# Kernel tuning notes

Measured on AMD Instinct MI355X. Metric: run time of the kernel, lower is better.

## Reference

```python
import jax, jax.numpy as jnp
import numpy as np

NEG_SLOPE = 0.2

def edge_softmax(logits, dst, num_nodes):
    # logits: [E, H]; softmax over incoming edges of each dst node, per head
    m = jax.ops.segment_max(logits, dst, num_segments=num_nodes)  # [N, H]
    e = jnp.exp(logits - m[dst])
    s = jax.ops.segment_sum(e, dst, num_segments=num_nodes)  # [N, H]
    return e / s[dst]

def gat_layer(h, src, dst, W, al, ar, b, activation):
    # W: [F_in, H*D], al/ar: [H, D], b: [H, D]
    N = h.shape[0]
    H, D = al.shape
    feat = (h @ W).reshape(N, H, D)
    el = jnp.sum(feat * al, axis=-1)  # [N, H]
    er = jnp.sum(feat * ar, axis=-1)  # [N, H]
    e = jax.nn.leaky_relu(el[src] + er[dst], NEG_SLOPE)  # [E, H]
    a = edge_softmax(e, dst, N)  # [E, H]
    msg = feat[src] * a[:, :, None]  # [E, H, D]
    rst = jax.ops.segment_sum(msg, dst, num_segments=N) + b[None]  # [N, H, D]
    if activation:
        rst = jax.nn.relu(rst)
    return rst

def setup_inputs() -> dict:
    key = jax.random.key(0)
    ks = jax.random.split(key, 16)
    N, E = 50000, 800000
    IN, HID, OUT, H = 128, 64, 64, 4
    s = 0.1
    return {
        "features": jax.random.normal(ks[0], (N, IN), jnp.float32),
        "src": jax.random.randint(ks[1], (E,), 0, N),
        "dst": jax.random.randint(ks[2], (E,), 0, N),
        "W1": jax.random.normal(ks[3], (IN, H * HID), jnp.float32) * s,
        "al1": jax.random.normal(ks[4], (H, HID), jnp.float32) * s,
        "ar1": jax.random.normal(ks[5], (H, HID), jnp.float32) * s,
        "b1": jnp.zeros((H, HID), jnp.float32),
        "W2": jax.random.normal(ks[6], (H * HID, H * HID), jnp.float32) * s,
        "al2": jax.random.normal(ks[7], (H, HID), jnp.float32) * s,
        "ar2": jax.random.normal(ks[8], (H, HID), jnp.float32) * s,
        "b2": jnp.zeros((H, HID), jnp.float32),
        "W3": jax.random.normal(ks[9], (H * HID, OUT), jnp.float32) * s,
        "al3": jax.random.normal(ks[10], (1, OUT), jnp.float32) * s,
        "ar3": jax.random.normal(ks[11], (1, OUT), jnp.float32) * s,
        "b3": jnp.zeros((1, OUT), jnp.float32),
    }

def reference(features, src, dst, W1, al1, ar1, b1, W2, al2, ar2, b2, W3, al3, ar3, b3):
    N = features.shape[0]
    h = gat_layer(features, src, dst, W1, al1, ar1, b1, activation=True)   # [N, 4, 64]
    h = h.reshape(N, -1)                                                    # [N, 256]
    h = gat_layer(h, src, dst, W2, al2, ar2, b2, activation=True)          # [N, 4, 64]
    h = h.reshape(N, -1)                                                    # [N, 256]
    h = gat_layer(h, src, dst, W3, al3, ar3, b3, activation=False)         # [N, 1, 64]
    return h.mean(axis=1)                                                   # [N, 64]
```

## Files before the change

### kernel.cpp

```cpp
#include <hip/hip_runtime.h>
#include <hip/hip_bf16.h>

#define LEAKY 0.2f

typedef __attribute__((ext_vector_type(8))) short short8;
typedef __attribute__((ext_vector_type(4))) float f32x4;

__device__ inline unsigned short f2b(float f) {
    unsigned u = __float_as_uint(f);
    u += 0x7FFFu + ((u >> 16) & 1u);
    return (unsigned short)(u >> 16);
}
__device__ inline float b2f(unsigned short s) {
    return __uint_as_float(((unsigned)s) << 16);
}


__global__ void k_prep(const float* __restrict__ features, unsigned short* __restrict__ fconv,
                       int n4,
                       const float* __restrict__ W1, const float* __restrict__ W2,
                       const float* __restrict__ W3, unsigned short* __restrict__ Wt1,
                       unsigned short* __restrict__ Wt2, unsigned short* __restrict__ Wt3,
                       int* __restrict__ bcnt) {
    int idx = blockIdx.x * blockDim.x + threadIdx.x;
    if (idx < n4) {
        float4 v = *(const float4*)(features + idx * 4);
        ushort4 o;
        o.x = f2b(v.x); o.y = f2b(v.y); o.z = f2b(v.z); o.w = f2b(v.w);
        *(ushort4*)(fconv + idx * 4) = o;
        return;
    }
    int j = idx - n4;
    if (j < 32768) {
        int m = j >> 7, k = j & 127;
        Wt1[j] = f2b(W1[(size_t)k * 256 + m]);
        return;
    }
    if (j < 98304) {
        int jj = j - 32768;
        int m = jj >> 8, k = jj & 255;
        Wt2[jj] = f2b(W2[(size_t)k * 256 + m]);
        return;
    }
    if (j < 114688) {
        int jj = j - 98304;
        int m = jj >> 8, k = jj & 255;
        Wt3[jj] = f2b(W3[(size_t)k * 64 + m]);
        return;
    }
    int z = j - 114688;
    if (z < 256) bcnt[z] = 0;
}


#define NEB 8192

__global__ __launch_bounds__(256)
void k_bin_count(const int* __restrict__ dst, int* __restrict__ bcnt, int E, int N) {
    __shared__ int lc[256];
    const int tid = threadIdx.x;
    lc[tid] = 0;
    __syncthreads();
    const int b0 = blockIdx.x * NEB;
    const int cnt = min(NEB, E - b0);
    for (int j = 0; j < NEB / 256; ++j) {
        int idx = j * 256 + tid;
        if (idx < cnt) {
            int dn = dst[b0 + idx];
            if ((unsigned)dn < (unsigned)N) atomicAdd(&lc[dn >> 8], 1);
        }
    }
    __syncthreads();
    if (lc[tid] > 0) atomicAdd(&bcnt[tid], lc[tid]);
}

__global__ __launch_bounds__(256)
void k_bucket_scan(const int* __restrict__ bcnt, int* __restrict__ bbase,
                   int* __restrict__ bcur, int* __restrict__ row_start_N, int B, int E) {
    __shared__ int ws[4];
    const int tid = threadIdx.x, lane = tid & 63, wave = tid >> 6;
    int v = (tid < B) ? bcnt[tid] : 0;
    int x = v;
    #pragma unroll
    for (int off = 1; off < 64; off <<= 1) {
        int t = __shfl_up(x, off, 64);
        if (lane >= off) x += t;
    }
    if (lane == 63) ws[wave] = x;
    __syncthreads();
    if (tid == 0) {
        int c = 0;
        #pragma unroll
        for (int wv = 0; wv < 4; ++wv) { int t = ws[wv]; ws[wv] = c; c += t; }
    }
    __syncthreads();
    int excl = x - v + ws[wave];
    if (tid < B) { bbase[tid] = excl; bcur[tid] = excl; }
    if (tid == 0) { bbase[B] = E; *row_start_N = E; }
}

__global__ __launch_bounds__(256)
void k_bin_scatter(const int* __restrict__ dst, int* __restrict__ bcur,
                   int* __restrict__ ebuf, int E, int N) {
    __shared__ int lc[256], lofs[256], lcur[256], gres[256];
    __shared__ int stage_e[NEB];
    __shared__ unsigned short stage_d[NEB];
    __shared__ int ws[4];
    const int tid = threadIdx.x, lane = tid & 63, wave = tid >> 6;
    const int b0 = blockIdx.x * NEB;
    const int cnt = min(NEB, E - b0);
    lc[tid] = 0;
    __syncthreads();

    int dreg[NEB / 256];
    #pragma unroll
    for (int j = 0; j < NEB / 256; ++j) {
        int idx = j * 256 + tid;
        dreg[j] = -1;
        if (idx < cnt) {
            int dn = dst[b0 + idx];
            if ((unsigned)dn < (unsigned)N) {
                dreg[j] = dn;
                atomicAdd(&lc[dn >> 8], 1);
            }
        }
    }
    __syncthreads();
    {
        int v = lc[tid];
        int x = v;
        #pragma unroll
        for (int off = 1; off < 64; off <<= 1) {
            int t = __shfl_up(x, off, 64);
            if (lane >= off) x += t;
        }
        if (lane == 63) ws[wave] = x;
        __syncthreads();
        if (tid == 0) {
            int c = 0;
            #pragma unroll
            for (int wv = 0; wv < 4; ++wv) { int t = ws[wv]; ws[wv] = c; c += t; }
        }
        __syncthreads();
        int excl = x - v + ws[wave];
        lofs[tid] = excl;
        lcur[tid] = excl;
    }
    __syncthreads();
    #pragma unroll
    for (int j = 0; j < NEB / 256; ++j) {
        int dn = dreg[j];
        if (dn >= 0) {
            int p = atomicAdd(&lcur[dn >> 8], 1);
            stage_e[p] = b0 + j * 256 + tid;
            stage_d[p] = (unsigned short)dn;
        }
    }
    __syncthreads();
    if (lc[tid] > 0) gres[tid] = atomicAdd(&bcur[tid], lc[tid]);
    __syncthreads();
    int total = lcur[255];
    for (int i = tid; i < total; i += 256) {
        int dn = stage_d[i];
        int k = dn >> 8;
        int dest = gres[k] + (i - lofs[k]);
        ebuf[dest] = ((dn & 255) << 24) | stage_e[i];
    }
}

__global__ __launch_bounds__(256)
void k_csr_build(const int* __restrict__ ebuf, const int* __restrict__ src,
                 const int* __restrict__ bbase, int* __restrict__ row_start,
                 int* __restrict__ src_sorted, int N) {
    __shared__ int lc[256], lcur[256];
    __shared__ int ws[4];
    const int tid = threadIdx.x, lane = tid & 63, wave = tid >> 6;
    const int k = blockIdx.x;
    const int base = k << 8;
    const int e0 = bbase[k];
    const int cnt = bbase[k + 1] - e0;
    lc[tid] = 0;
    __syncthreads();
    for (int i = tid; i < cnt; i += 256) {
        int rel = ((unsigned)ebuf[e0 + i]) >> 24;
        atomicAdd(&lc[rel], 1);
    }
    __syncthreads();
    {
        int v = lc[tid];
        int x = v;
        #pragma unroll
        for (int off = 1; off < 64; off <<= 1) {
            int t = __shfl_up(x, off, 64);
            if (lane >= off) x += t;
        }
        if (lane == 63) ws[wave] = x;
        __syncthreads();
        if (tid == 0) {
            int c = 0;
            #pragma unroll
            for (int wv = 0; wv < 4; ++wv) { int t = ws[wv]; ws[wv] = c; c += t; }
        }
        __syncthreads();
        int excl = x - v + ws[wave];
        lcur[tid] = excl;
        int n = base + tid;
        if (n < N) row_start[n] = e0 + excl;
    }
    __syncthreads();
    for (int i = tid; i < cnt; i += 256) {
        int val = ebuf[e0 + i];
        int rel = ((unsigned)val) >> 24;
        int e = val & 0xFFFFFF;
        int p = atomicAdd(&lcur[rel], 1);
        src_sorted[e0 + p] = src[e];
    }
}


__global__ __launch_bounds__(256)
void k_gemm_mfma(const unsigned short* __restrict__ A, const unsigned short* __restrict__ Wt,
                 unsigned short* __restrict__ Cb, const float* __restrict__ al,
                 const float* __restrict__ ar, float* __restrict__ el,
                 float* __restrict__ er, int N, int K, int M) {
    constexpr int STR = 40;
    __shared__ unsigned short As[128 * STR];
    __shared__ unsigned short Bs[128 * STR];
    const int tid  = threadIdx.x;
    const int wave = tid >> 6;
    const int lane = tid & 63;
    const int row0 = blockIdx.y * 128;
    const int col0 = blockIdx.x * 128;
    const int wr = (wave >> 1) * 64;
    const int wc = (wave & 1) * 64;
    const int m16 = lane & 15;
    const int q   = lane >> 4;

    const int s_row = tid >> 1;
    const int s_off = (tid & 1) * 16;

    f32x4 acc[4][4] = {};

    for (int k0 = 0; k0 < K; k0 += 32) {
        {
            int gr = row0 + s_row;
            short8 z = {};
            short8 v0 = z, v1 = z;
            if (gr < N) {
                const unsigned short* ap = A + (size_t)gr * K + k0 + s_off;
                v0 = *(const short8*)ap;
                v1 = *(const short8*)(ap + 8);
            }
            *(short8*)&As[s_row * STR + s_off]     = v0;
            *(short8*)&As[s_row * STR + s_off + 8] = v1;
        }
        {
            const unsigned short* sp = Wt + (size_t)(col0 + s_row) * K + k0 + s_off;
            *(short8*)&Bs[s_row * STR + s_off]     = *(const short8*)sp;
            *(short8*)&Bs[s_row * STR + s_off + 8] = *(const short8*)(sp + 8);
        }
        __syncthreads();

        short8 afr[4], bfr[4];
        #pragma unroll
        for (int rg = 0; rg < 4; ++rg)
            afr[rg] = *(const short8*)&As[(wr + rg * 16 + m16) * STR + q * 8];
        #pragma unroll
        for (int cg = 0; cg < 4; ++cg)
            bfr[cg] = *(const short8*)&Bs[(wc + cg * 16 + m16) * STR + q * 8];
        #pragma unroll
        for (int rg = 0; rg < 4; ++rg)
            #pragma unroll
            for (int cg = 0; cg < 4; ++cg)
                acc[rg][cg] = __builtin_amdgcn_mfma_f32_16x16x32_bf16(
                    afr[rg], bfr[cg], acc[rg][cg], 0, 0, 0);
        __syncthreads();
    }

    const int H = M >> 6;
    const int h = (col0 + wc) >> 6;
    float alv[4], arv[4];
    #pragma unroll
    for (int cg = 0; cg < 4; ++cg) {
        alv[cg] = al[h * 64 + cg * 16 + m16];
        arv[cg] = ar[h * 64 + cg * 16 + m16];
    }

    #pragma unroll
    for (int rg = 0; rg < 4; ++rg) {
        #pragma unroll
        for (int r = 0; r < 4; ++r) {
            int gr = row0 + wr + rg * 16 + q * 4 + r;
            float pl = 0.f, pr = 0.f;
            #pragma unroll
            for (int cg = 0; cg < 4; ++cg) {
                pl = fmaf(acc[rg][cg][r], alv[cg], pl);
                pr = fmaf(acc[rg][cg][r], arv[cg], pr);
            }
            #pragma unroll
            for (int off = 1; off < 16; off <<= 1) {
                pl += __shfl_xor(pl, off, 64);
                pr += __shfl_xor(pr, off, 64);
            }
            if (gr < N) {
                unsigned short* bp = Cb + (size_t)gr * M + col0 + wc + m16;
                #pragma unroll
                for (int cg = 0; cg < 4; ++cg)
                    bp[cg * 16] = f2b(acc[rg][cg][r]);
                if (m16 == 0) {
                    el[gr * H + h] = pl;
                    er[gr * H + h] = pr;
                }
            }
        }
    }
}


__global__ __launch_bounds__(256)
void k_gemm_mfma64(const unsigned short* __restrict__ A, const unsigned short* __restrict__ Wt,
                   unsigned short* __restrict__ Cb, const float* __restrict__ al,
                   const float* __restrict__ ar, float* __restrict__ el,
                   float* __restrict__ er, int N, int K) {
    constexpr int M = 64;
    constexpr int STR = 40;
    __shared__ unsigned short As[256 * STR];
    __shared__ unsigned short Bs[64 * STR];
    const int tid  = threadIdx.x;
    const int wave = tid >> 6;
    const int lane = tid & 63;
    const int row0 = blockIdx.x * 256;
    const int wr = wave * 64;
    const int m16 = lane & 15;
    const int q   = lane >> 4;

    const int s_row = tid >> 1;
    const int s_off = (tid & 1) * 16;
    const int b_row = tid >> 2;
    const int b_chk = (tid & 3) * 8;

    f32x4 acc[4][4] = {};

    for (int k0 = 0; k0 < K; k0 += 32) {
        #pragma unroll
        for (int p = 0; p < 2; ++p) {
            int r = s_row + p * 128;
            int gr = row0 + r;
            short8 z = {};
            short8 v0 = z, v1 = z;
            if (gr < N) {
                const unsigned short* ap = A + (size_t)gr * K + k0 + s_off;
                v0 = *(const short8*)ap;
                v1 = *(const short8*)(ap + 8);
            }
            *(short8*)&As[r * STR + s_off]     = v0;
            *(short8*)&As[r * STR + s_off + 8] = v1;
        }
        {
            const unsigned short* sp = Wt + (size_t)b_row * K + k0 + b_chk;
            *(short8*)&Bs[b_row * STR + b_chk] = *(const short8*)sp;
        }
        __syncthreads();

        short8 afr[4], bfr[4];
        #pragma unroll
        for (int rg = 0; rg < 4; ++rg)
            afr[rg] = *(const short8*)&As[(wr + rg * 16 + m16) * STR + q * 8];
        #pragma unroll
        for (int cg = 0; cg < 4; ++cg)
            bfr[cg] = *(const short8*)&Bs[(cg * 16 + m16) * STR + q * 8];
        #pragma unroll
        for (int rg = 0; rg < 4; ++rg)
            #pragma unroll
            for (int cg = 0; cg < 4; ++cg)
                acc[rg][cg] = __builtin_amdgcn_mfma_f32_16x16x32_bf16(
                    afr[rg], bfr[cg], acc[rg][cg], 0, 0, 0);
        __syncthreads();
    }

    float alv[4], arv[4];
    #pragma unroll
    for (int cg = 0; cg < 4; ++cg) {
        alv[cg] = al[cg * 16 + m16];
        arv[cg] = ar[cg * 16 + m16];
    }

    #pragma unroll
    for (int rg = 0; rg < 4; ++rg) {
        #pragma unroll
        for (int r = 0; r < 4; ++r) {
            int gr = row0 + wr + rg * 16 + q * 4 + r;
            float pl = 0.f, pr = 0.f;
            #pragma unroll
            for (int cg = 0; cg < 4; ++cg) {
                pl = fmaf(acc[rg][cg][r], alv[cg], pl);
                pr = fmaf(acc[rg][cg][r], arv[cg], pr);
            }
            #pragma unroll
            for (int off = 1; off < 16; off <<= 1) {
                pl += __shfl_xor(pl, off, 64);
                pr += __shfl_xor(pr, off, 64);
            }
            if (gr < N) {
                unsigned short* bp = Cb + (size_t)gr * M + m16;
                #pragma unroll
                for (int cg = 0; cg < 4; ++cg)
                    bp[cg * 16] = f2b(acc[rg][cg][r]);
                if (m16 == 0) {
                    el[gr] = pl;
                    er[gr] = pr;
                }
            }
        }
    }
}


template<int H>
__global__ __launch_bounds__(256)
void k_node_msw(const int* __restrict__ row_start, const int* __restrict__ src_sorted,
                const float* __restrict__ el, const float* __restrict__ er,
                float* __restrict__ w, unsigned short* __restrict__ wb,
                float* __restrict__ s, int N, int E) {
    constexpr int STRIDE = 64 / H;
    constexpr int CAP = 64;
    constexpr int LSTR = 65;
    __shared__ float ldsw[4 * H * LSTR];
    const int wv = threadIdx.x >> 6;
    const int n = blockIdx.x * 4 + wv;
    if (n >= N) return;
    const int lane = threadIdx.x & 63;
    const int eo = lane / H;
    const int h  = lane % H;
    float* lw = &ldsw[(wv * H + h) * LSTR];
    float erv = er[n * H + h];
    int b0 = row_start[n], b1 = row_start[n + 1];
    float mx = -INFINITY;
    for (int i = b0 + eo; i < b1; i += STRIDE) {
        float x = el[src_sorted[i] * H + h] + erv;
        x = (x > 0.f) ? x : LEAKY * x;
        int j = i - b0;
        if (j < CAP) lw[j] = x;
        else w[(size_t)h * E + i] = x;
        mx = fmaxf(mx, x);
    }
    #pragma unroll
    for (int off = H; off < 64; off <<= 1)
        mx = fmaxf(mx, __shfl_xor(mx, off, 64));
    float sum = 0.f;
    for (int i = b0 + eo; i < b1; i += STRIDE) {
        int j = i - b0;
        float x = (j < CAP) ? lw[j] : w[(size_t)h * E + i];
        float e = __expf(x - mx);
        sum += e;
        wb[(size_t)h * E + i] = f2b(e);
    }
    #pragma unroll
    for (int off = H; off < 64; off <<= 1)
        sum += __shfl_xor(sum, off, 64);
    if (lane < H) s[n * H + lane] = 1.0f / fmaxf(sum, 1e-30f);
}

template<int OUTBF>
__global__ __launch_bounds__(256)
void k_agg_b(const int* __restrict__ row_start, const int* __restrict__ src_sorted,
             const uint4* __restrict__ featp, const unsigned short* __restrict__ wb,
             const float* __restrict__ s, const float* __restrict__ bias,
             void* __restrict__ outv, int H, int N, int E, int do_relu) {
    const int M = H * 64;
    const int P = M >> 3;
    const int G = 256 / P;
    const int grp = threadIdx.x / P;
    const int t = threadIdx.x - grp * P;
    const int n = blockIdx.x * G + grp;
    if (n >= N) return;
    const int d0 = t * 8;
    const int h = d0 >> 6;
    const unsigned short* wh = wb + (size_t)h * E;

    float a[8] = {};
    int b0 = row_start[n], b1 = row_start[n + 1];
    int i = b0;
    for (; i + 8 <= b1; i += 8) {
        int ss[8]; float wv[8]; uint4 pv[8];
        #pragma unroll
        for (int j = 0; j < 8; ++j) ss[j] = src_sorted[i + j];
        #pragma unroll
        for (int j = 0; j < 8; ++j) wv[j] = b2f(wh[i + j]);
        #pragma unroll
        for (int j = 0; j < 8; ++j) pv[j] = featp[(size_t)ss[j] * P + t];
        #pragma unroll
        for (int j = 0; j < 8; ++j) {
            a[0] = fmaf(__uint_as_float(pv[j].x << 16),         wv[j], a[0]);
            a[1] = fmaf(__uint_as_float(pv[j].x & 0xFFFF0000u), wv[j], a[1]);
            a[2] = fmaf(__uint_as_float(pv[j].y << 16),         wv[j], a[2]);
            a[3] = fmaf(__uint_as_float(pv[j].y & 0xFFFF0000u), wv[j], a[3]);
            a[4] = fmaf(__uint_as_float(pv[j].z << 16),         wv[j], a[4]);
            a[5] = fmaf(__uint_as_float(pv[j].z & 0xFFFF0000u), wv[j], a[5]);
            a[6] = fmaf(__uint_as_float(pv[j].w << 16),         wv[j], a[6]);
            a[7] = fmaf(__uint_as_float(pv[j].w & 0xFFFF0000u), wv[j], a[7]);
        }
    }
    for (; i + 4 <= b1; i += 4) {
        int ss[4]; float wv[4]; uint4 pv[4];
        #pragma unroll
        for (int j = 0; j < 4; ++j) ss[j] = src_sorted[i + j];
        #pragma unroll
        for (int j = 0; j < 4; ++j) wv[j] = b2f(wh[i + j]);
        #pragma unroll
        for (int j = 0; j < 4; ++j) pv[j] = featp[(size_t)ss[j] * P + t];
        #pragma unroll
        for (int j = 0; j < 4; ++j) {
            a[0] = fmaf(__uint_as_float(pv[j].x << 16),         wv[j], a[0]);
            a[1] = fmaf(__uint_as_float(pv[j].x & 0xFFFF0000u), wv[j], a[1]);
            a[2] = fmaf(__uint_as_float(pv[j].y << 16),         wv[j], a[2]);
            a[3] = fmaf(__uint_as_float(pv[j].y & 0xFFFF0000u), wv[j], a[3]);
            a[4] = fmaf(__uint_as_float(pv[j].z << 16),         wv[j], a[4]);
            a[5] = fmaf(__uint_as_float(pv[j].z & 0xFFFF0000u), wv[j], a[5]);
            a[6] = fmaf(__uint_as_float(pv[j].w << 16),         wv[j], a[6]);
            a[7] = fmaf(__uint_as_float(pv[j].w & 0xFFFF0000u), wv[j], a[7]);
        }
    }
    for (; i < b1; ++i) {
        uint4 pv = featp[(size_t)src_sorted[i] * P + t];
        float wv = b2f(wh[i]);
        a[0] = fmaf(__uint_as_float(pv.x << 16),         wv, a[0]);
        a[1] = fmaf(__uint_as_float(pv.x & 0xFFFF0000u), wv, a[1]);
        a[2] = fmaf(__uint_as_float(pv.y << 16),         wv, a[2]);
        a[3] = fmaf(__uint_as_float(pv.y & 0xFFFF0000u), wv, a[3]);
        a[4] = fmaf(__uint_as_float(pv.z << 16),         wv, a[4]);
        a[5] = fmaf(__uint_as_float(pv.z & 0xFFFF0000u), wv, a[5]);
        a[6] = fmaf(__uint_as_float(pv.w << 16),         wv, a[6]);
        a[7] = fmaf(__uint_as_float(pv.w & 0xFFFF0000u), wv, a[7]);
    }
    float rs = s[n * H + h];
    float4 bv0 = *(const float4*)(bias + d0);
    float4 bv1 = *(const float4*)(bias + d0 + 4);
    a[0] = fmaf(a[0], rs, bv0.x); a[1] = fmaf(a[1], rs, bv0.y);
    a[2] = fmaf(a[2], rs, bv0.z); a[3] = fmaf(a[3], rs, bv0.w);
    a[4] = fmaf(a[4], rs, bv1.x); a[5] = fmaf(a[5], rs, bv1.y);
    a[6] = fmaf(a[6], rs, bv1.z); a[7] = fmaf(a[7], rs, bv1.w);
    if (do_relu) {
        #pragma unroll
        for (int j = 0; j < 8; ++j) a[j] = fmaxf(a[j], 0.f);
    }
    if (OUTBF) {
        uint4 o;
        o.x = (unsigned)f2b(a[0]) | ((unsigned)f2b(a[1]) << 16);
        o.y = (unsigned)f2b(a[2]) | ((unsigned)f2b(a[3]) << 16);
        o.z = (unsigned)f2b(a[4]) | ((unsigned)f2b(a[5]) << 16);
        o.w = (unsigned)f2b(a[6]) | ((unsigned)f2b(a[7]) << 16);
        *(uint4*)((unsigned short*)outv + (size_t)n * M + d0) = o;
    } else {
        *(float4*)((float*)outv + (size_t)n * M + d0)     = make_float4(a[0], a[1], a[2], a[3]);
        *(float4*)((float*)outv + (size_t)n * M + d0 + 4) = make_float4(a[4], a[5], a[6], a[7]);
    }
}


static void run_layer(const unsigned short* A, int K, const unsigned short* Wt,
                      const float* al_, const float* ar_, const float* b_, int H,
                      unsigned short* featb, void* rstOut, bool outBf,
                      float* el, float* er, float* w, unsigned short* wb, float* s,
                      const int* row_start, const int* src_sorted,
                      int N, int E, bool do_relu, hipStream_t stream) {
    const int M = H * 64;
    if (M % 128 == 0) {
        dim3 gg(M / 128, (N + 127) / 128);
        k_gemm_mfma<<<gg, 256, 0, stream>>>(A, Wt, featb, al_, ar_, el, er, N, K, M);
    } else {
        k_gemm_mfma64<<<(N + 255) / 256, 256, 0, stream>>>(A, Wt, featb, al_, ar_, el, er, N, K);
    }

    if (H == 4)
        k_node_msw<4><<<(N + 3) / 4, 256, 0, stream>>>(row_start, src_sorted, el, er, w, wb, s, N, E);
    else
        k_node_msw<1><<<(N + 3) / 4, 256, 0, stream>>>(row_start, src_sorted, el, er, w, wb, s, N, E);

    int G = 256 / (M / 8);
    if (outBf)
        k_agg_b<1><<<(N + G - 1) / G, 256, 0, stream>>>(row_start, src_sorted,
                                                        (const uint4*)featb, wb, s,
                                                        b_, rstOut, H, N, E, do_relu ? 1 : 0);
    else
        k_agg_b<0><<<(N + G - 1) / G, 256, 0, stream>>>(row_start, src_sorted,
                                                        (const uint4*)featb, wb, s,
                                                        b_, rstOut, H, N, E, do_relu ? 1 : 0);
}

extern "C" void kernel_launch(void* const* d_in, const int* in_sizes, int n_in,
                              void* d_out, int out_size, void* d_ws, size_t ws_size,
                              hipStream_t stream) {
    const float* features = (const float*)d_in[0];
    const int*   src = (const int*)d_in[1];
    const int*   dst = (const int*)d_in[2];
    const float* W1  = (const float*)d_in[3];
    const float* al1 = (const float*)d_in[4];
    const float* ar1 = (const float*)d_in[5];
    const float* b1  = (const float*)d_in[6];
    const float* W2  = (const float*)d_in[7];
    const float* al2 = (const float*)d_in[8];
    const float* ar2 = (const float*)d_in[9];
    const float* b2  = (const float*)d_in[10];
    const float* W3  = (const float*)d_in[11];
    const float* al3 = (const float*)d_in[12];
    const float* ar3 = (const float*)d_in[13];
    const float* b3  = (const float*)d_in[14];

    const int N = in_sizes[0] / 128;
    const int E = in_sizes[1];
    const int B = (N + 255) >> 8;
    const int n4 = N * 128 / 4;

    float* ws   = (float*)d_ws;
    float* el   = ws;
    float* er   = el + (size_t)N * 4;
    float* s    = er + (size_t)N * 4;
    float* w    = s  + (size_t)N * 4;
    unsigned short* wb = (unsigned short*)(w + (size_t)E * 4);
    int* row_start  = (int*)(wb + (size_t)E * 4);
    int* src_sorted = row_start + N + 1;
    int* ebuf       = src_sorted + E;
    int* bcnt       = ebuf + E;
    int* bbase      = bcnt + 256;
    int* bcur       = bbase + 257;
    uintptr_t wp = (uintptr_t)(bcur + 256);
    wp = (wp + 15) & ~(uintptr_t)15;
    unsigned short* Wt1   = (unsigned short*)wp;
    unsigned short* Wt2   = Wt1 + 32768;
    unsigned short* Wt3   = Wt2 + 65536;
    unsigned short* fconv = Wt3 + 16384;
    unsigned short* featb = fconv + (size_t)N * 128;
    unsigned short* rstb  = featb + (size_t)N * 256;

    int prep_total = n4 + 114688 + 256;
    k_prep<<<(prep_total + 255) / 256, 256, 0, stream>>>(features, fconv, n4,
                                                         W1, W2, W3, Wt1, Wt2, Wt3, bcnt);

    int nbb = (E + NEB - 1) / NEB;
    k_bin_count<<<nbb, 256, 0, stream>>>(dst, bcnt, E, N);
    k_bucket_scan<<<1, 256, 0, stream>>>(bcnt, bbase, bcur, row_start + N, B, E);
    k_bin_scatter<<<nbb, 256, 0, stream>>>(dst, bcur, ebuf, E, N);
    k_csr_build<<<B, 256, 0, stream>>>(ebuf, src, bbase, row_start, src_sorted, N);

    run_layer(fconv, 128, Wt1, al1, ar1, b1, 4, featb, rstb, true,
              el, er, w, wb, s, row_start, src_sorted, N, E, true, stream);
    run_layer(rstb, 256, Wt2, al2, ar2, b2, 4, featb, rstb, true,
              el, er, w, wb, s, row_start, src_sorted, N, E, true, stream);
    run_layer(rstb, 256, Wt3, al3, ar3, b3, 1, featb, d_out, false,
              el, er, w, wb, s, row_start, src_sorted, N, E, false, stream);
}
```

Before: 422.3 us.

## Fuse edge softmax into aggregation kernel using monotone max of el

Removes the separate per-node softmax kernel and computes the max from the max of el over incoming edges plus er, passed through leaky-relu, which is exact by monotonicity. The aggregation kernel now gathers el, computes the exp weights and their sum inline, and normalizes at the end. This eliminates the intermediate weight and inverse-sum buffers and one launch per layer. In exchange, every thread in a node group recomputes the exps, and el is gathered twice.

```diff
diff --git a/kernel.cpp b/kernel.cpp
--- a/kernel.cpp
+++ b/kernel.cpp
@@ -415,58 +415,12 @@
     }
 }
 
-
-template<int H>
-__global__ __launch_bounds__(256)
-void k_node_msw(const int* __restrict__ row_start, const int* __restrict__ src_sorted,
-                const float* __restrict__ el, const float* __restrict__ er,
-                float* __restrict__ w, unsigned short* __restrict__ wb,
-                float* __restrict__ s, int N, int E) {
-    constexpr int STRIDE = 64 / H;
-    constexpr int CAP = 64;
-    constexpr int LSTR = 65;
-    __shared__ float ldsw[4 * H * LSTR];
-    const int wv = threadIdx.x >> 6;
-    const int n = blockIdx.x * 4 + wv;
-    if (n >= N) return;
-    const int lane = threadIdx.x & 63;
-    const int eo = lane / H;
-    const int h  = lane % H;
-    float* lw = &ldsw[(wv * H + h) * LSTR];
-    float erv = er[n * H + h];
-    int b0 = row_start[n], b1 = row_start[n + 1];
-    float mx = -INFINITY;
-    for (int i = b0 + eo; i < b1; i += STRIDE) {
-        float x = el[src_sorted[i] * H + h] + erv;
-        x = (x > 0.f) ? x : LEAKY * x;
-        int j = i - b0;
-        if (j < CAP) lw[j] = x;
-        else w[(size_t)h * E + i] = x;
-        mx = fmaxf(mx, x);
-    }
-    #pragma unroll
-    for (int off = H; off < 64; off <<= 1)
-        mx = fmaxf(mx, __shfl_xor(mx, off, 64));
-    float sum = 0.f;
-    for (int i = b0 + eo; i < b1; i += STRIDE) {
-        int j = i - b0;
-        float x = (j < CAP) ? lw[j] : w[(size_t)h * E + i];
-        float e = __expf(x - mx);
-        sum += e;
-        wb[(size_t)h * E + i] = f2b(e);
-    }
-    #pragma unroll
-    for (int off = H; off < 64; off <<= 1)
-        sum += __shfl_xor(sum, off, 64);
-    if (lane < H) s[n * H + lane] = 1.0f / fmaxf(sum, 1e-30f);
-}
-
 template<int OUTBF>
 __global__ __launch_bounds__(256)
-void k_agg_b(const int* __restrict__ row_start, const int* __restrict__ src_sorted,
-             const uint4* __restrict__ featp, const unsigned short* __restrict__ wb,
-             const float* __restrict__ s, const float* __restrict__ bias,
-             void* __restrict__ outv, int H, int N, int E, int do_relu) {
+void k_agg_f(const int* __restrict__ row_start, const int* __restrict__ src_sorted,
+             const uint4* __restrict__ featp, const float* __restrict__ el,
+             const float* __restrict__ er, const float* __restrict__ bias,
+             void* __restrict__ outv, int H, int N, int do_relu) {
     const int M = H * 64;
     const int P = M >> 3;
     const int G = 256 / P;
@@ -476,19 +430,38 @@
     if (n >= N) return;
     const int d0 = t * 8;
     const int h = d0 >> 6;
-    const unsigned short* wh = wb + (size_t)h * E;
+    const float erv = er[n * H + h];
+
+    const int b0 = row_start[n], b1 = row_start[n + 1];
+
+    float mxe = -INFINITY;
+    for (int i = b0 + (t & 7); i < b1; i += 8)
+        mxe = fmaxf(mxe, el[(size_t)src_sorted[i] * H + h]);
+    mxe = fmaxf(mxe, __shfl_xor(mxe, 1, 64));
+    mxe = fmaxf(mxe, __shfl_xor(mxe, 2, 64));
+    mxe = fmaxf(mxe, __shfl_xor(mxe, 4, 64));
+    float mx = mxe + erv;
+    mx = (mx > 0.f) ? mx : LEAKY * mx;
 
     float a[8] = {};
-    int b0 = row_start[n], b1 = row_start[n + 1];
+    float sum = 0.f;
     int i = b0;
     for (; i + 8 <= b1; i += 8) {
         int ss[8]; float wv[8]; uint4 pv[8];
         #pragma unroll
         for (int j = 0; j < 8; ++j) ss[j] = src_sorted[i + j];
         #pragma unroll
-        for (int j = 0; j < 8; ++j) wv[j] = b2f(wh[i + j]);
+        for (int j = 0; j < 8; ++j) wv[j] = el[(size_t)ss[j] * H + h];
         #pragma unroll
         for (int j = 0; j < 8; ++j) pv[j] = featp[(size_t)ss[j] * P + t];
+        #pragma unroll
+        for (int j = 0; j < 8; ++j) {
+            float x = wv[j] + erv;
+            x = (x > 0.f) ? x : LEAKY * x;
+            float w = __expf(x - mx);
+            wv[j] = w;
+            sum += w;
+        }
         #pragma unroll
         for (int j = 0; j < 8; ++j) {
             a[0] = fmaf(__uint_as_float(pv[j].x << 16),         wv[j], a[0]);
@@ -506,9 +479,17 @@
         #pragma unroll
         for (int j = 0; j < 4; ++j) ss[j] = src_sorted[i + j];
         #pragma unroll
-        for (int j = 0; j < 4; ++j) wv[j] = b2f(wh[i + j]);
+        for (int j = 0; j < 4; ++j) wv[j] = el[(size_t)ss[j] * H + h];
         #pragma unroll
         for (int j = 0; j < 4; ++j) pv[j] = featp[(size_t)ss[j] * P + t];
+        #pragma unroll
+        for (int j = 0; j < 4; ++j) {
+            float x = wv[j] + erv;
+            x = (x > 0.f) ? x : LEAKY * x;
+            float w = __expf(x - mx);
+            wv[j] = w;
+            sum += w;
+        }
         #pragma unroll
         for (int j = 0; j < 4; ++j) {
             a[0] = fmaf(__uint_as_float(pv[j].x << 16),         wv[j], a[0]);
@@ -522,18 +503,23 @@
         }
     }
     for (; i < b1; ++i) {
-        uint4 pv = featp[(size_t)src_sorted[i] * P + t];
-        float wv = b2f(wh[i]);
-        a[0] = fmaf(__uint_as_float(pv.x << 16),         wv, a[0]);
-        a[1] = fmaf(__uint_as_float(pv.x & 0xFFFF0000u), wv, a[1]);
-        a[2] = fmaf(__uint_as_float(pv.y << 16),         wv, a[2]);
-        a[3] = fmaf(__uint_as_float(pv.y & 0xFFFF0000u), wv, a[3]);
-        a[4] = fmaf(__uint_as_float(pv.z << 16),         wv, a[4]);
-        a[5] = fmaf(__uint_as_float(pv.z & 0xFFFF0000u), wv, a[5]);
-        a[6] = fmaf(__uint_as_float(pv.w << 16),         wv, a[6]);
-        a[7] = fmaf(__uint_as_float(pv.w & 0xFFFF0000u), wv, a[7]);
-    }
-    float rs = s[n * H + h];
+        int ss = src_sorted[i];
+        float x = el[(size_t)ss * H + h] + erv;
+        uint4 pv = featp[(size_t)ss * P + t];
+        x = (x > 0.f) ? x : LEAKY * x;
+        float w = __expf(x - mx);
+        sum += w;
+        a[0] = fmaf(__uint_as_float(pv.x << 16),         w, a[0]);
+        a[1] = fmaf(__uint_as_float(pv.x & 0xFFFF0000u), w, a[1]);
+        a[2] = fmaf(__uint_as_float(pv.y << 16),         w, a[2]);
+        a[3] = fmaf(__uint_as_float(pv.y & 0xFFFF0000u), w, a[3]);
+        a[4] = fmaf(__uint_as_float(pv.z << 16),         w, a[4]);
+        a[5] = fmaf(__uint_as_float(pv.z & 0xFFFF0000u), w, a[5]);
+        a[6] = fmaf(__uint_as_float(pv.w << 16),         w, a[6]);
+        a[7] = fmaf(__uint_as_float(pv.w & 0xFFFF0000u), w, a[7]);
+    }
+
+    float rs = 1.0f / fmaxf(sum, 1e-30f);
     float4 bv0 = *(const float4*)(bias + d0);
     float4 bv1 = *(const float4*)(bias + d0 + 4);
     a[0] = fmaf(a[0], rs, bv0.x); a[1] = fmaf(a[1], rs, bv0.y);
@@ -561,7 +547,7 @@
 static void run_layer(const unsigned short* A, int K, const unsigned short* Wt,
                       const float* al_, const float* ar_, const float* b_, int H,
                       unsigned short* featb, void* rstOut, bool outBf,
-                      float* el, float* er, float* w, unsigned short* wb, float* s,
+                      float* el, float* er,
                       const int* row_start, const int* src_sorted,
                       int N, int E, bool do_relu, hipStream_t stream) {
     const int M = H * 64;
@@ -572,20 +558,15 @@
         k_gemm_mfma64<<<(N + 255) / 256, 256, 0, stream>>>(A, Wt, featb, al_, ar_, el, er, N, K);
     }
 
-    if (H == 4)
-        k_node_msw<4><<<(N + 3) / 4, 256, 0, stream>>>(row_start, src_sorted, el, er, w, wb, s, N, E);
-    else
-        k_node_msw<1><<<(N + 3) / 4, 256, 0, stream>>>(row_start, src_sorted, el, er, w, wb, s, N, E);
-
     int G = 256 / (M / 8);
     if (outBf)
-        k_agg_b<1><<<(N + G - 1) / G, 256, 0, stream>>>(row_start, src_sorted,
-                                                        (const uint4*)featb, wb, s,
-                                                        b_, rstOut, H, N, E, do_relu ? 1 : 0);
+        k_agg_f<1><<<(N + G - 1) / G, 256, 0, stream>>>(row_start, src_sorted,
+                                                        (const uint4*)featb, el, er,
+                                                        b_, rstOut, H, N, do_relu ? 1 : 0);
     else
-        k_agg_b<0><<<(N + G - 1) / G, 256, 0, stream>>>(row_start, src_sorted,
-                                                        (const uint4*)featb, wb, s,
-                                                        b_, rstOut, H, N, E, do_relu ? 1 : 0);
+        k_agg_f<0><<<(N + G - 1) / G, 256, 0, stream>>>(row_start, src_sorted,
+                                                        (const uint4*)featb, el, er,
+                                                        b_, rstOut, H, N, do_relu ? 1 : 0);
 }
 
 extern "C" void kernel_launch(void* const* d_in, const int* in_sizes, int n_in,
@@ -615,10 +596,7 @@
     float* ws   = (float*)d_ws;
     float* el   = ws;
     float* er   = el + (size_t)N * 4;
-    float* s    = er + (size_t)N * 4;
-    float* w    = s  + (size_t)N * 4;
-    unsigned short* wb = (unsigned short*)(w + (size_t)E * 4);
-    int* row_start  = (int*)(wb + (size_t)E * 4);
+    int* row_start  = (int*)(er + (size_t)N * 4);
     int* src_sorted = row_start + N + 1;
     int* ebuf       = src_sorted + E;
     int* bcnt       = ebuf + E;
@@ -644,9 +622,9 @@
     k_csr_build<<<B, 256, 0, stream>>>(ebuf, src, bbase, row_start, src_sorted, N);
 
     run_layer(fconv, 128, Wt1, al1, ar1, b1, 4, featb, rstb, true,
-              el, er, w, wb, s, row_start, src_sorted, N, E, true, stream);
+              el, er, row_start, src_sorted, N, E, true, stream);
     run_layer(rstb, 256, Wt2, al2, ar2, b2, 4, featb, rstb, true,
-              el, er, w, wb, s, row_start, src_sorted, N, E, true, stream);
+              el, er, row_start, src_sorted, N, E, true, stream);
     run_layer(rstb, 256, Wt3, al3, ar3, b3, 1, featb, d_out, false,
-              el, er, w, wb, s, row_start, src_sorted, N, E, false, stream);
-}
+              el, er, row_start, src_sorted, N, E, false, stream);
+}
```

Measured after the change: 401.4 us. -4.9%, faster.
